# Kernel optimization log

Hardware: AMD Instinct MI355X
Metric: run time of the kernel (lower is better)

## Reference

```python
import jax, jax.numpy as jnp
import numpy as np
from jax import lax

T, B, E, H, V, TAGS = 256, 64, 1024, 1024, 50000, 50


def setup_inputs() -> dict:
    key = jax.random.key(0)
    ks = jax.random.split(key, 16)
    s = 0.02
    return {
        "X": jax.random.randint(ks[0], (T, B), 0, V),
        "lengths": jnp.full((B,), T, dtype=jnp.int64 if jax.config.jax_enable_x64 else jnp.int32),
        "embedding": jax.random.normal(ks[1], (V, E), dtype=jnp.float32) * s,
        "w_ih": jax.random.normal(ks[2], (H, E), dtype=jnp.float32) * s,
        "w_hh": jax.random.normal(ks[3], (H, H), dtype=jnp.float32) * s,
        "w_ch": jax.random.normal(ks[4], (H, H), dtype=jnp.float32) * s,
        "w_c2h": jax.random.normal(ks[5], (H, H), dtype=jnp.float32) * s,
        "b_ih": jax.random.normal(ks[6], (H,), dtype=jnp.float32) * s,
        "b_hh": jax.random.normal(ks[7], (H,), dtype=jnp.float32) * s,
        "b_ch": jax.random.normal(ks[8], (H,), dtype=jnp.float32) * s,
        "b_c2h": jax.random.normal(ks[9], (H,), dtype=jnp.float32) * s,
        "dense_w": jax.random.normal(ks[10], (TAGS, H), dtype=jnp.float32) * s,
        "dense_b": jax.random.normal(ks[11], (TAGS,), dtype=jnp.float32) * s,
        "h0": jax.random.normal(ks[12], (B, H), dtype=jnp.float32),
        "c0": jax.random.normal(ks[13], (B, H), dtype=jnp.float32),
    }


def reference(X, lengths, embedding, w_ih, w_hh, w_ch, w_c2h,
              b_ih, b_hh, b_ch, b_c2h, dense_w, dense_b, h0, c0):
    # Embedding lookup: X is time-major [T, B] -> emb [T, B, E]
    emb = embedding[X]

    def step(carry, x_t):
        hx, cx = carry
        pre = x_t @ w_ih.T + b_ih + hx @ w_hh.T + b_hh          # [B, H]
        # In the source, ingate and forgetgate are identical expressions
        gate_if = jax.nn.sigmoid(pre + cx @ w_ch.T + b_ch)
        cellgate = jnp.tanh(pre)
        cy = gate_if * cx + gate_if * cellgate
        outgate = jax.nn.sigmoid(pre + cy @ w_c2h.T + b_c2h)
        hy = outgate * jnp.tanh(cy)
        return (hy, cy), hy

    _, out = lax.scan(step, (h0, c0), emb)                       # out: [T, B, H]
    flat = out.reshape(-1, out.shape[-1])                        # [T*B, H]
    # dropout_rate=0 / eval mode -> identity
    logits = flat @ dense_w.T + dense_b                          # [T*B, TAGS]
    return jax.nn.softmax(logits, axis=1)
```

## Files before the change

kernel.cpp:

```cpp
#include <hip/hip_runtime.h>
#include <hip/hip_cooperative_groups.h>

typedef __bf16 bf16;
typedef __bf16 bf16x8 __attribute__((ext_vector_type(8)));
typedef float f32x4 __attribute__((ext_vector_type(4)));
typedef unsigned int u32;
typedef unsigned long long u64;
typedef unsigned int u32x4 __attribute__((ext_vector_type(4)));

#define TT 256
#define NTAGS 50

#define OFF_WIH   0ull
#define OFF_WHH   2097152ull
#define OFF_WCH   4194304ull
#define OFF_WC2H  6291456ull
#define OFF_DW    8388608ull
#define OFF_XW    8519680ull
#define OFF_HISTB 42074112ull
#define OFF_HB    75628544ull
#define OFF_CB    75890688ull
#define OFF_BAR   76152832ull
#define N_FLAG_WORDS (4 * 64 * 32)

__device__ __forceinline__ u64 cohload(const u64* p) {
  return __hip_atomic_load(p, __ATOMIC_RELAXED, __HIP_MEMORY_SCOPE_AGENT);
}
__device__ __forceinline__ void cohstore(u64* p, u64 v) {
  __hip_atomic_store(p, v, __ATOMIC_RELAXED, __HIP_MEMORY_SCOPE_AGENT);
}
__device__ __forceinline__ u32x4 cohload_q4(const bf16* p) {
  union { u64 q[2]; u32x4 v; } u;
  const u64* q = (const u64*)p;
  u.q[0] = cohload(q);
  u.q[1] = cohload(q + 1);
  return u.v;
}

__global__ void k_prep(const float* __restrict__ wih, const float* __restrict__ whh,
                       const float* __restrict__ wch, const float* __restrict__ wc2h,
                       const float* __restrict__ dw, const float* __restrict__ h0,
                       const float* __restrict__ c0, char* __restrict__ ws) {
  const long N_W = 4194304, N_DW = 65536, N_S = 65536;
  const long TOT = N_W + N_DW + 2 * N_S + N_FLAG_WORDS;
  long stride = (long)gridDim.x * blockDim.x;
  for (long idx = (long)blockIdx.x * blockDim.x + threadIdx.x; idx < TOT; idx += stride) {
    if (idx < N_W) {
      long m = idx >> 20, e = idx & 1048575;
      const float* s = (m == 0) ? wih : (m == 1) ? whh : (m == 2) ? wch : wc2h;
      ((bf16*)(ws + OFF_WIH))[idx] = (bf16)s[e];
    } else if (idx < N_W + N_DW) {
      long j = idx - N_W; long r = j >> 10, e = j & 1023;
      ((bf16*)(ws + OFF_DW))[j] = (bf16)((r < NTAGS) ? dw[r * 1024 + e] : 0.f);
    } else if (idx < N_W + N_DW + N_S) {
      long j = idx - N_W - N_DW;
      ((bf16*)(ws + OFF_HB))[j] = (bf16)h0[j];
    } else if (idx < N_W + N_DW + 2 * N_S) {
      long j = idx - N_W - N_DW - N_S;
      ((bf16*)(ws + OFF_CB))[j] = (bf16)c0[j];
    } else {
      long j = idx - N_W - N_DW - 2 * N_S;
      ((u32*)(ws + OFF_BAR))[j] = 0u;
    }
  }
}

__global__ __launch_bounds__(256, 1) void k_xw(const int* __restrict__ X,
                                               const float* __restrict__ emb,
                                               const float* __restrict__ b_ih,
                                               const float* __restrict__ b_hh,
                                               char* __restrict__ ws) {
  const bf16* wih = (const bf16*)(ws + OFF_WIH);
  bf16* xw = (bf16*)(ws + OFF_XW);
  int l = threadIdx.x & 63, wv = threadIdx.x >> 6;
  int i0 = blockIdx.x * 64 + wv * 16;
  const float* ap = emb + (long)X[i0 + (l & 15)] * 1024 + ((l >> 4) * 8);

  bf16x8 a_reg[32];
#pragma unroll
  for (int k = 0; k < 32; ++k) {
    f32x4 f0 = *(const f32x4*)(ap + k * 32);
    f32x4 f1 = *(const f32x4*)(ap + k * 32 + 4);
    bf16x8 a;
#pragma unroll
    for (int q = 0; q < 4; ++q) { a[q] = (bf16)f0[q]; a[4 + q] = (bf16)f1[q]; }
    a_reg[k] = a;
  }

  f32x4 zero = {0.f, 0.f, 0.f, 0.f};
  for (int ct = 0; ct < 16; ++ct) {
    int h0 = ct * 64;
    const bf16* bp = wih + (long)(h0 + (l & 15)) * 1024 + ((l >> 4) * 8);
    f32x4 acc[4] = {zero, zero, zero, zero};
#pragma unroll
    for (int k = 0; k < 32; ++k)
#pragma unroll
      for (int j = 0; j < 4; ++j) {
        bf16x8 b = *(const bf16x8*)(bp + j * 16 * 1024 + k * 32);
        acc[j] = __builtin_amdgcn_mfma_f32_16x16x32_bf16(a_reg[k], b, acc[j], 0, 0, 0);
      }
#pragma unroll
    for (int j = 0; j < 4; ++j)
#pragma unroll
      for (int r = 0; r < 4; ++r) {
        int row = i0 + (l >> 4) * 4 + r;
        int col = h0 + j * 16 + (l & 15);
        xw[(long)row * 1024 + col] = (bf16)(acc[j][r] + b_ih[col] + b_hh[col]);
      }
  }
}

__global__ __launch_bounds__(256, 1) void k_rnn(const float* __restrict__ b_ch,
                                                const float* __restrict__ b_c2h,
                                                const float* __restrict__ c0,
                                                char* __restrict__ ws) {
  const bf16* xw = (const bf16*)(ws + OFF_XW);
  bf16* histb = (bf16*)(ws + OFF_HISTB);
  bf16* HB = (bf16*)(ws + OFF_HB);
  bf16* CB = (bf16*)(ws + OFF_CB);
  int g = blockIdx.x & 3, j = blockIdx.x >> 2;
  u32* flags = (u32*)(ws + OFF_BAR) + g * 64 * 32;

  int l = threadIdx.x & 63, wv = threadIdx.x >> 6;
  int b0 = g * 16, h0b = j * 16;
  int e = threadIdx.x;
  int eoff = (b0 + (e >> 4)) * 1024 + h0b + (e & 15);
  int gh = h0b + (e & 15);

  __shared__ float red[4][2][256];
  __shared__ bf16 xfer[256];

  int lane_r = l & 15;
  int koff = wv * 256 + ((l >> 4) * 8);
  long arow = (long)(b0 + lane_r) * 1024 + koff;
  int hp = l >> 5;

  u32x4 whh_r[8], wch_r[8], wc2h_r[8], cfr[8];
  {
    const bf16* p1 = (const bf16*)(ws + OFF_WHH)  + (long)(h0b + lane_r) * 1024 + koff;
    const bf16* p2 = (const bf16*)(ws + OFF_WCH)  + (long)(h0b + lane_r) * 1024 + koff;
    const bf16* p3 = (const bf16*)(ws + OFF_WC2H) + (long)(h0b + lane_r) * 1024 + koff;
#pragma unroll
    for (int kk = 0; kk < 8; ++kk) {
      whh_r[kk]  = *(const u32x4*)(p1 + kk * 32);
      wch_r[kk]  = *(const u32x4*)(p2 + kk * 32);
      wc2h_r[kk] = *(const u32x4*)(p3 + kk * 32);
      cfr[kk] = cohload_q4(CB + arow + kk * 32);
    }
  }

  float bch_v = b_ch[gh], bc2h_v = b_c2h[gh];
  float c_reg = c0[eoff];
  f32x4 zero = {0.f, 0.f, 0.f, 0.f};

  for (int t = 0; t < TT; ++t) {
    asm volatile("" : "+v"(whh_r[0]), "+v"(whh_r[1]), "+v"(whh_r[2]), "+v"(whh_r[3]),
                      "+v"(whh_r[4]), "+v"(whh_r[5]), "+v"(whh_r[6]), "+v"(whh_r[7]),
                      "+v"(wch_r[0]), "+v"(wch_r[1]), "+v"(wch_r[2]), "+v"(wch_r[3]),
                      "+v"(wch_r[4]), "+v"(wch_r[5]), "+v"(wch_r[6]), "+v"(wch_r[7]));
    asm volatile("" : "+v"(wc2h_r[0]), "+v"(wc2h_r[1]), "+v"(wc2h_r[2]), "+v"(wc2h_r[3]),
                      "+v"(wc2h_r[4]), "+v"(wc2h_r[5]), "+v"(wc2h_r[6]), "+v"(wc2h_r[7]));
    asm volatile("" : "+v"(cfr[0]), "+v"(cfr[1]), "+v"(cfr[2]), "+v"(cfr[3]),
                      "+v"(cfr[4]), "+v"(cfr[5]), "+v"(cfr[6]), "+v"(cfr[7]));

    long slot1 = (long)((t + 1) & 1) * 65536;
    float xwv = (float)xw[(long)t * 65536 + eoff];
    u32 tkH = 2u * t;
    u32 tkA = 2u * t + 1u, tkB = 2u * t + 2u;

    f32x4 ap_ = zero, ac_ = zero;
    u32x4 hfr[8];
    {
      const bf16* hx = HB + (long)(t & 1) * 65536;
#pragma unroll
      for (int kk = 0; kk < 8; ++kk) {
        const u32* fp = &flags[(wv * 16 + kk * 2 + hp) * 32];
        while (!__all(__hip_atomic_load(fp, __ATOMIC_RELAXED, __HIP_MEMORY_SCOPE_AGENT) >= tkH))
          __builtin_amdgcn_s_sleep(1);
        hfr[kk] = cohload_q4(hx + arow + kk * 32);
        ac_ = __builtin_amdgcn_mfma_f32_16x16x32_bf16(
            __builtin_bit_cast(bf16x8, cfr[kk]), __builtin_bit_cast(bf16x8, wch_r[kk]), ac_, 0, 0, 0);
      }
    }
    asm volatile("" ::: "memory");
#pragma unroll
    for (int kk = 0; kk < 8; ++kk)
      ap_ = __builtin_amdgcn_mfma_f32_16x16x32_bf16(
          __builtin_bit_cast(bf16x8, hfr[kk]), __builtin_bit_cast(bf16x8, whh_r[kk]), ap_, 0, 0, 0);
#pragma unroll
    for (int r = 0; r < 4; ++r) {
      int ei = ((l >> 4) * 4 + r) * 16 + (l & 15);
      red[wv][0][ei] = ap_[r];
      red[wv][1][ei] = ac_[r];
    }
    __syncthreads();
    float pre = red[0][0][e] + red[1][0][e] + red[2][0][e] + red[3][0][e] + xwv;
    float cgm = red[0][1][e] + red[1][1][e] + red[2][1][e] + red[3][1][e] + bch_v;
    float gif = 1.f / (1.f + expf(-(pre + cgm)));
    float cy = gif * (c_reg + tanhf(pre));
    c_reg = cy;
    xfer[e] = (bf16)cy;
    __syncthreads();
    if (e < 64)
      cohstore((u64*)(CB + slot1 + (long)(b0 + (e >> 2)) * 1024 + h0b) + (e & 3),
               ((u64*)xfer)[e]);
    asm volatile("s_waitcnt vmcnt(0)" ::: "memory");
    if (e == 0)
      __hip_atomic_store(&flags[j * 32], tkA, __ATOMIC_RELAXED, __HIP_MEMORY_SCOPE_AGENT);

    {
      const bf16* cyp = CB + slot1;
#pragma unroll
      for (int kk = 0; kk < 8; ++kk) {
        const u32* fp = &flags[(wv * 16 + kk * 2 + hp) * 32];
        while (!__all(__hip_atomic_load(fp, __ATOMIC_RELAXED, __HIP_MEMORY_SCOPE_AGENT) >= tkA))
          __builtin_amdgcn_s_sleep(1);
        cfr[kk] = cohload_q4(cyp + arow + kk * 32);
      }
    }
    asm volatile("" ::: "memory");
    f32x4 ao = zero;
#pragma unroll
    for (int kk = 0; kk < 8; ++kk)
      ao = __builtin_amdgcn_mfma_f32_16x16x32_bf16(
          __builtin_bit_cast(bf16x8, cfr[kk]), __builtin_bit_cast(bf16x8, wc2h_r[kk]), ao, 0, 0, 0);
#pragma unroll
    for (int r = 0; r < 4; ++r)
      red[wv][0][((l >> 4) * 4 + r) * 16 + (l & 15)] = ao[r];
    __syncthreads();
    float o = red[0][0][e] + red[1][0][e] + red[2][0][e] + red[3][0][e] + bc2h_v;
    float og = 1.f / (1.f + expf(-(pre + o)));
    bf16 hb = (bf16)(og * tanhf(cy));
    xfer[e] = hb;
    __syncthreads();
    if (t < TT - 1) {
      if (e < 64)
        cohstore((u64*)(HB + slot1 + (long)(b0 + (e >> 2)) * 1024 + h0b) + (e & 3),
                 ((u64*)xfer)[e]);
      asm volatile("s_waitcnt vmcnt(0)" ::: "memory");
      if (e == 0)
        __hip_atomic_store(&flags[j * 32], tkB, __ATOMIC_RELAXED, __HIP_MEMORY_SCOPE_AGENT);
    }
    histb[(long)t * 65536 + eoff] = hb;
  }
}

__global__ __launch_bounds__(256) void k_out(const float* __restrict__ dense_b,
                                             const char* __restrict__ ws,
                                             float* __restrict__ out) {
  const bf16* h  = (const bf16*)(ws + OFF_HISTB);
  const bf16* dw = (const bf16*)(ws + OFF_DW);
  int l = threadIdx.x & 63, wv = threadIdx.x >> 6;
  int i0 = blockIdx.x * 64 + wv * 16;
  const bf16* ap = h  + (long)(i0 + (l & 15)) * 1024 + ((l >> 4) * 8);
  const bf16* bp = dw + (long)(l & 15) * 1024 + ((l >> 4) * 8);
  f32x4 zero = {0.f, 0.f, 0.f, 0.f};
  f32x4 acc[4] = {zero, zero, zero, zero};
  for (int k = 0; k < 1024; k += 32) {
    bf16x8 a = *(const bf16x8*)(ap + k);
#pragma unroll
    for (int j = 0; j < 4; ++j) {
      bf16x8 b = *(const bf16x8*)(bp + j * 16 * 1024 + k);
      acc[j] = __builtin_amdgcn_mfma_f32_16x16x32_bf16(a, b, acc[j], 0, 0, 0);
    }
  }
  int tag0 = l & 15;
#pragma unroll
  for (int r = 0; r < 4; ++r) {
    int row = i0 + (l >> 4) * 4 + r;
    float lg[4], ex[4];
    float mx = -1e30f;
#pragma unroll
    for (int j = 0; j < 4; ++j) {
      int tag = j * 16 + tag0;
      lg[j] = (tag < NTAGS) ? (acc[j][r] + dense_b[tag]) : -1e30f;
      mx = fmaxf(mx, lg[j]);
    }
    for (int m = 1; m < 16; m <<= 1) mx = fmaxf(mx, __shfl_xor(mx, m, 64));
    float s = 0.f;
#pragma unroll
    for (int j = 0; j < 4; ++j) {
      int tag = j * 16 + tag0;
      ex[j] = (tag < NTAGS) ? expf(lg[j] - mx) : 0.f;
      s += ex[j];
    }
    for (int m = 1; m < 16; m <<= 1) s += __shfl_xor(s, m, 64);
    float inv = 1.f / s;
#pragma unroll
    for (int j = 0; j < 4; ++j) {
      int tag = j * 16 + tag0;
      if (tag < NTAGS) out[(long)row * 50 + tag] = ex[j] * inv;
    }
  }
}

extern "C" void kernel_launch(void* const* d_in, const int* in_sizes, int n_in,
                              void* d_out, int out_size, void* d_ws, size_t ws_size,
                              hipStream_t stream) {
  const int*   X        = (const int*)d_in[0];
  const float* embedding = (const float*)d_in[2];
  const float* w_ih  = (const float*)d_in[3];
  const float* w_hh  = (const float*)d_in[4];
  const float* w_ch  = (const float*)d_in[5];
  const float* w_c2h = (const float*)d_in[6];
  const float* b_ih  = (const float*)d_in[7];
  const float* b_hh  = (const float*)d_in[8];
  const float* b_ch  = (const float*)d_in[9];
  const float* b_c2h = (const float*)d_in[10];
  const float* dense_w = (const float*)d_in[11];
  const float* dense_b = (const float*)d_in[12];
  const float* h0 = (const float*)d_in[13];
  const float* c0 = (const float*)d_in[14];
  char* ws = (char*)d_ws;
  float* out = (float*)d_out;

  k_prep<<<2048, 256, 0, stream>>>(w_ih, w_hh, w_ch, w_c2h, dense_w, h0, c0, ws);
  k_xw<<<256, 256, 0, stream>>>(X, embedding, b_ih, b_hh, ws);

  void* args[] = {(void*)&b_ch, (void*)&b_c2h, (void*)&c0, (void*)&ws};
  hipLaunchCooperativeKernel((const void*)k_rnn, dim3(256), dim3(256), args, 0, stream);

  k_out<<<256, 256, 0, stream>>>(dense_b, ws, out);
}
```

Measured before the change: 2.556 ms.

## Use single-wave RNN blocks with full-K MFMA per wave, dropping LDS reduction

The recurrent kernel now runs 64 threads per block, and each wave covers the whole K=1024 dimension. This removes the cross-wave LDS reduction and the __syncthreads barriers inside each timestep. Weights are no longer held in registers but streamed from global/L2 every step, while the c-state fragments (32 quads) stay resident. The precomputed input projection is stored in MFMA fragment order as packed u64, so each lane does one coalesced load per step. Each step is now serial over 32 MFMAs per matrix per wave, with heavy weight reloads from cache and high register pressure.

```diff
diff --git a/kernel.cpp b/kernel.cpp
--- a/kernel.cpp
+++ b/kernel.cpp
@@ -4,6 +4,7 @@
 typedef __bf16 bf16;
 typedef __bf16 bf16x8 __attribute__((ext_vector_type(8)));
 typedef float f32x4 __attribute__((ext_vector_type(4)));
+typedef unsigned short u16;
 typedef unsigned int u32;
 typedef unsigned long long u64;
 typedef unsigned int u32x4 __attribute__((ext_vector_type(4)));
@@ -35,6 +36,13 @@
   u.q[0] = cohload(q);
   u.q[1] = cohload(q + 1);
   return u.v;
+}
+__device__ __forceinline__ float bf2f(u32 bits) {
+  return __builtin_bit_cast(float, bits << 16);
+}
+__device__ __forceinline__ void lds_fence() {
+  asm volatile("s_waitcnt lgkmcnt(0)" ::: "memory");
+  __builtin_amdgcn_sched_barrier(0);
 }
 
 __global__ void k_prep(const float* __restrict__ wih, const float* __restrict__ whh,
@@ -71,7 +79,7 @@
                                                const float* __restrict__ b_hh,
                                                char* __restrict__ ws) {
   const bf16* wih = (const bf16*)(ws + OFF_WIH);
-  bf16* xw = (bf16*)(ws + OFF_XW);
+  u64* xwA = (u64*)(ws + OFF_XW);
   int l = threadIdx.x & 63, wv = threadIdx.x >> 6;
   int i0 = blockIdx.x * 64 + wv * 16;
   const float* ap = emb + (long)X[i0 + (l & 15)] * 1024 + ((l >> 4) * 8);
@@ -88,6 +96,7 @@
   }
 
   f32x4 zero = {0.f, 0.f, 0.f, 0.f};
+  long rowtile = (long)blockIdx.x * 4 + wv;
   for (int ct = 0; ct < 16; ++ct) {
     int h0 = ct * 64;
     const bf16* bp = wih + (long)(h0 + (l & 15)) * 1024 + ((l >> 4) * 8);
@@ -100,148 +109,147 @@
         acc[j] = __builtin_amdgcn_mfma_f32_16x16x32_bf16(a_reg[k], b, acc[j], 0, 0, 0);
       }
 #pragma unroll
-    for (int j = 0; j < 4; ++j)
-#pragma unroll
-      for (int r = 0; r < 4; ++r) {
-        int row = i0 + (l >> 4) * 4 + r;
-        int col = h0 + j * 16 + (l & 15);
-        xw[(long)row * 1024 + col] = (bf16)(acc[j][r] + b_ih[col] + b_hh[col]);
-      }
-  }
-}
-
-__global__ __launch_bounds__(256, 1) void k_rnn(const float* __restrict__ b_ch,
-                                                const float* __restrict__ b_c2h,
-                                                const float* __restrict__ c0,
-                                                char* __restrict__ ws) {
-  const bf16* xw = (const bf16*)(ws + OFF_XW);
+    for (int j = 0; j < 4; ++j) {
+      int col = h0 + j * 16 + (l & 15);
+      float bias = b_ih[col] + b_hh[col];
+      u64 pk = 0;
+#pragma unroll
+      for (int r = 0; r < 4; ++r)
+        pk |= (u64)__builtin_bit_cast(u16, (bf16)(acc[j][r] + bias)) << (16 * r);
+      xwA[(rowtile * 64 + (ct * 4 + j)) * 64 + l] = pk;
+    }
+  }
+}
+
+__global__ __launch_bounds__(64, 1) void k_rnn(const float* __restrict__ b_ch,
+                                               const float* __restrict__ b_c2h,
+                                               const float* __restrict__ c0,
+                                               char* __restrict__ ws) {
+  const u64* xwA = (const u64*)(ws + OFF_XW);
   bf16* histb = (bf16*)(ws + OFF_HISTB);
   bf16* HB = (bf16*)(ws + OFF_HB);
   bf16* CB = (bf16*)(ws + OFF_CB);
   int g = blockIdx.x & 3, j = blockIdx.x >> 2;
   u32* flags = (u32*)(ws + OFF_BAR) + g * 64 * 32;
 
-  int l = threadIdx.x & 63, wv = threadIdx.x >> 6;
-  int b0 = g * 16, h0b = j * 16;
-  int e = threadIdx.x;
-  int eoff = (b0 + (e >> 4)) * 1024 + h0b + (e & 15);
-  int gh = h0b + (e & 15);
-
-  __shared__ float red[4][2][256];
-  __shared__ bf16 xfer[256];
-
-  int lane_r = l & 15;
-  int koff = wv * 256 + ((l >> 4) * 8);
-  long arow = (long)(b0 + lane_r) * 1024 + koff;
-  int hp = l >> 5;
-
-  u32x4 whh_r[8], wch_r[8], wc2h_r[8], cfr[8];
-  {
-    const bf16* p1 = (const bf16*)(ws + OFF_WHH)  + (long)(h0b + lane_r) * 1024 + koff;
-    const bf16* p2 = (const bf16*)(ws + OFF_WCH)  + (long)(h0b + lane_r) * 1024 + koff;
-    const bf16* p3 = (const bf16*)(ws + OFF_WC2H) + (long)(h0b + lane_r) * 1024 + koff;
-#pragma unroll
-    for (int kk = 0; kk < 8; ++kk) {
-      whh_r[kk]  = *(const u32x4*)(p1 + kk * 32);
-      wch_r[kk]  = *(const u32x4*)(p2 + kk * 32);
-      wc2h_r[kk] = *(const u32x4*)(p3 + kk * 32);
-      cfr[kk] = cohload_q4(CB + arow + kk * 32);
-    }
-  }
-
-  float bch_v = b_ch[gh], bc2h_v = b_c2h[gh];
-  float c_reg = c0[eoff];
+  int l = threadIdx.x;
+  int b0 = g * 16, n0 = j * 16;
+  int lane_r = l & 15, k8 = (l >> 4) * 8;
+  long arow = (long)(b0 + lane_r) * 1024 + k8;
+  long wrow = (long)(n0 + lane_r) * 1024 + k8;
+  const bf16* whh  = (const bf16*)(ws + OFF_WHH)  + wrow;
+  const bf16* wch  = (const bf16*)(ws + OFF_WCH)  + wrow;
+  const bf16* wc2h = (const bf16*)(ws + OFF_WC2H) + wrow;
+
+  __shared__ u16 xfs[256];
+
+  int er = l >> 4, ec = l & 15;
+  float c_reg[4];
+#pragma unroll
+  for (int r = 0; r < 4; ++r)
+    c_reg[r] = c0[(b0 + er * 4 + r) * 1024 + n0 + ec];
+  float bch_v = b_ch[n0 + ec], bc2h_v = b_c2h[n0 + ec];
   f32x4 zero = {0.f, 0.f, 0.f, 0.f};
 
+  u32x4 cfr[32];
+#pragma unroll
+  for (int kk = 0; kk < 32; ++kk)
+    cfr[kk] = cohload_q4(CB + arow + kk * 32);
+
+  int srow = l >> 2, scol = (l & 3) * 4;
+
   for (int t = 0; t < TT; ++t) {
-    asm volatile("" : "+v"(whh_r[0]), "+v"(whh_r[1]), "+v"(whh_r[2]), "+v"(whh_r[3]),
-                      "+v"(whh_r[4]), "+v"(whh_r[5]), "+v"(whh_r[6]), "+v"(whh_r[7]),
-                      "+v"(wch_r[0]), "+v"(wch_r[1]), "+v"(wch_r[2]), "+v"(wch_r[3]),
-                      "+v"(wch_r[4]), "+v"(wch_r[5]), "+v"(wch_r[6]), "+v"(wch_r[7]));
-    asm volatile("" : "+v"(wc2h_r[0]), "+v"(wc2h_r[1]), "+v"(wc2h_r[2]), "+v"(wc2h_r[3]),
-                      "+v"(wc2h_r[4]), "+v"(wc2h_r[5]), "+v"(wc2h_r[6]), "+v"(wc2h_r[7]));
-    asm volatile("" : "+v"(cfr[0]), "+v"(cfr[1]), "+v"(cfr[2]), "+v"(cfr[3]),
-                      "+v"(cfr[4]), "+v"(cfr[5]), "+v"(cfr[6]), "+v"(cfr[7]));
-
+    u32 tkH = 2u * t, tkA = 2u * t + 1u, tkB = 2u * t + 2u;
     long slot1 = (long)((t + 1) & 1) * 65536;
-    float xwv = (float)xw[(long)t * 65536 + eoff];
-    u32 tkH = 2u * t;
-    u32 tkA = 2u * t + 1u, tkB = 2u * t + 2u;
-
-    f32x4 ap_ = zero, ac_ = zero;
-    u32x4 hfr[8];
+    u64 xwp = xwA[((long)(t * 4 + g) * 64 + j) * 64 + l];
+
+    f32x4 c0a = zero, c1a = zero;
+#pragma unroll
+    for (int kk = 0; kk < 32; ++kk) {
+      u32x4 w = *(const u32x4*)(wch + kk * 32);
+      if (kk & 1)
+        c1a = __builtin_amdgcn_mfma_f32_16x16x32_bf16(
+            __builtin_bit_cast(bf16x8, cfr[kk]), __builtin_bit_cast(bf16x8, w), c1a, 0, 0, 0);
+      else
+        c0a = __builtin_amdgcn_mfma_f32_16x16x32_bf16(
+            __builtin_bit_cast(bf16x8, cfr[kk]), __builtin_bit_cast(bf16x8, w), c0a, 0, 0, 0);
+    }
+
     {
-      const bf16* hx = HB + (long)(t & 1) * 65536;
-#pragma unroll
-      for (int kk = 0; kk < 8; ++kk) {
-        const u32* fp = &flags[(wv * 16 + kk * 2 + hp) * 32];
-        while (!__all(__hip_atomic_load(fp, __ATOMIC_RELAXED, __HIP_MEMORY_SCOPE_AGENT) >= tkH))
-          __builtin_amdgcn_s_sleep(1);
-        hfr[kk] = cohload_q4(hx + arow + kk * 32);
-        ac_ = __builtin_amdgcn_mfma_f32_16x16x32_bf16(
-            __builtin_bit_cast(bf16x8, cfr[kk]), __builtin_bit_cast(bf16x8, wch_r[kk]), ac_, 0, 0, 0);
-      }
+      const u32* my = &flags[l * 32];
+      while (!__all(__hip_atomic_load(my, __ATOMIC_RELAXED, __HIP_MEMORY_SCOPE_AGENT) >= tkH))
+        __builtin_amdgcn_s_sleep(1);
     }
     asm volatile("" ::: "memory");
-#pragma unroll
-    for (int kk = 0; kk < 8; ++kk)
-      ap_ = __builtin_amdgcn_mfma_f32_16x16x32_bf16(
-          __builtin_bit_cast(bf16x8, hfr[kk]), __builtin_bit_cast(bf16x8, whh_r[kk]), ap_, 0, 0, 0);
+
+    const bf16* hx = HB + (long)(t & 1) * 65536 + arow;
+    f32x4 h0a = zero, h1a = zero;
+#pragma unroll
+    for (int kk = 0; kk < 32; ++kk) {
+      u32x4 hf = cohload_q4(hx + kk * 32);
+      u32x4 w = *(const u32x4*)(whh + kk * 32);
+      if (kk & 1)
+        h1a = __builtin_amdgcn_mfma_f32_16x16x32_bf16(
+            __builtin_bit_cast(bf16x8, hf), __builtin_bit_cast(bf16x8, w), h1a, 0, 0, 0);
+      else
+        h0a = __builtin_amdgcn_mfma_f32_16x16x32_bf16(
+            __builtin_bit_cast(bf16x8, hf), __builtin_bit_cast(bf16x8, w), h0a, 0, 0, 0);
+    }
+
+    float pre_s[4], cy_s[4];
 #pragma unroll
     for (int r = 0; r < 4; ++r) {
-      int ei = ((l >> 4) * 4 + r) * 16 + (l & 15);
-      red[wv][0][ei] = ap_[r];
-      red[wv][1][ei] = ac_[r];
-    }
-    __syncthreads();
-    float pre = red[0][0][e] + red[1][0][e] + red[2][0][e] + red[3][0][e] + xwv;
-    float cgm = red[0][1][e] + red[1][1][e] + red[2][1][e] + red[3][1][e] + bch_v;
-    float gif = 1.f / (1.f + expf(-(pre + cgm)));
-    float cy = gif * (c_reg + tanhf(pre));
-    c_reg = cy;
-    xfer[e] = (bf16)cy;
-    __syncthreads();
-    if (e < 64)
-      cohstore((u64*)(CB + slot1 + (long)(b0 + (e >> 2)) * 1024 + h0b) + (e & 3),
-               ((u64*)xfer)[e]);
+      float pre = h0a[r] + h1a[r] + bf2f((u32)(xwp >> (16 * r)) & 0xFFFFu);
+      float cgm = c0a[r] + c1a[r] + bch_v;
+      float gif = 1.f / (1.f + expf(-(pre + cgm)));
+      float cy = gif * (c_reg[r] + tanhf(pre));
+      c_reg[r] = cy;
+      pre_s[r] = pre;
+      cy_s[r] = cy;
+      xfs[(er * 4 + r) * 16 + ec] = __builtin_bit_cast(u16, (bf16)cy);
+    }
+    lds_fence();
+    u64 pkc = ((const u64*)xfs)[l];
+    cohstore((u64*)(CB + slot1 + (long)(b0 + srow) * 1024 + n0 + scol), pkc);
     asm volatile("s_waitcnt vmcnt(0)" ::: "memory");
-    if (e == 0)
+    if (l == 0)
       __hip_atomic_store(&flags[j * 32], tkA, __ATOMIC_RELAXED, __HIP_MEMORY_SCOPE_AGENT);
-
     {
-      const bf16* cyp = CB + slot1;
-#pragma unroll
-      for (int kk = 0; kk < 8; ++kk) {
-        const u32* fp = &flags[(wv * 16 + kk * 2 + hp) * 32];
-        while (!__all(__hip_atomic_load(fp, __ATOMIC_RELAXED, __HIP_MEMORY_SCOPE_AGENT) >= tkA))
-          __builtin_amdgcn_s_sleep(1);
-        cfr[kk] = cohload_q4(cyp + arow + kk * 32);
-      }
+      const u32* my = &flags[l * 32];
+      while (!__all(__hip_atomic_load(my, __ATOMIC_RELAXED, __HIP_MEMORY_SCOPE_AGENT) >= tkA))
+        __builtin_amdgcn_s_sleep(1);
     }
     asm volatile("" ::: "memory");
-    f32x4 ao = zero;
-#pragma unroll
-    for (int kk = 0; kk < 8; ++kk)
-      ao = __builtin_amdgcn_mfma_f32_16x16x32_bf16(
-          __builtin_bit_cast(bf16x8, cfr[kk]), __builtin_bit_cast(bf16x8, wc2h_r[kk]), ao, 0, 0, 0);
-#pragma unroll
-    for (int r = 0; r < 4; ++r)
-      red[wv][0][((l >> 4) * 4 + r) * 16 + (l & 15)] = ao[r];
-    __syncthreads();
-    float o = red[0][0][e] + red[1][0][e] + red[2][0][e] + red[3][0][e] + bc2h_v;
-    float og = 1.f / (1.f + expf(-(pre + o)));
-    bf16 hb = (bf16)(og * tanhf(cy));
-    xfer[e] = hb;
-    __syncthreads();
+
+    const bf16* cyp = CB + slot1 + arow;
+    f32x4 o0a = zero, o1a = zero;
+#pragma unroll
+    for (int kk = 0; kk < 32; ++kk) {
+      cfr[kk] = cohload_q4(cyp + kk * 32);
+      u32x4 w = *(const u32x4*)(wc2h + kk * 32);
+      if (kk & 1)
+        o1a = __builtin_amdgcn_mfma_f32_16x16x32_bf16(
+            __builtin_bit_cast(bf16x8, cfr[kk]), __builtin_bit_cast(bf16x8, w), o1a, 0, 0, 0);
+      else
+        o0a = __builtin_amdgcn_mfma_f32_16x16x32_bf16(
+            __builtin_bit_cast(bf16x8, cfr[kk]), __builtin_bit_cast(bf16x8, w), o0a, 0, 0, 0);
+    }
+#pragma unroll
+    for (int r = 0; r < 4; ++r) {
+      float o = o0a[r] + o1a[r] + bc2h_v;
+      float og = 1.f / (1.f + expf(-(pre_s[r] + o)));
+      float hy = og * tanhf(cy_s[r]);
+      xfs[(er * 4 + r) * 16 + ec] = __builtin_bit_cast(u16, (bf16)hy);
+    }
+    lds_fence();
+    u64 pkh = ((const u64*)xfs)[l];
+    *(u64*)(histb + (long)t * 65536 + (long)(b0 + srow) * 1024 + n0 + scol) = pkh;
     if (t < TT - 1) {
-      if (e < 64)
-        cohstore((u64*)(HB + slot1 + (long)(b0 + (e >> 2)) * 1024 + h0b) + (e & 3),
-                 ((u64*)xfer)[e]);
+      cohstore((u64*)(HB + slot1 + (long)(b0 + srow) * 1024 + n0 + scol), pkh);
       asm volatile("s_waitcnt vmcnt(0)" ::: "memory");
-      if (e == 0)
+      if (l == 0)
         __hip_atomic_store(&flags[j * 32], tkB, __ATOMIC_RELAXED, __HIP_MEMORY_SCOPE_AGENT);
     }
-    histb[(long)t * 65536 + eoff] = hb;
   }
 }
 
@@ -318,7 +326,7 @@
   k_xw<<<256, 256, 0, stream>>>(X, embedding, b_ih, b_hh, ws);
 
   void* args[] = {(void*)&b_ch, (void*)&b_c2h, (void*)&c0, (void*)&ws};
-  hipLaunchCooperativeKernel((const void*)k_rnn, dim3(256), dim3(256), args, 0, stream);
+  hipLaunchCooperativeKernel((const void*)k_rnn, dim3(256), dim3(64), args, 0, stream);
 
   k_out<<<256, 256, 0, stream>>>(dense_b, ws, out);
 }
```

After: 3.027 ms. +18.4%, slower.
